# Kernel optimization log

Measured on AMD Instinct MI355X. Metric: run time of the kernel, lower is better.

## Reference

```python
import jax, jax.numpy as jnp
import numpy as np

B, N, IN_DIM, SLOT_DIM, HIDDEN = 32, 4096, 256, 256, 512
NUM_SLOTS, NUM_ITERS = 8, 3
EPS_LN = 1e-5


def layernorm(x, g, b):
    m = jnp.mean(x, axis=-1, keepdims=True)
    v = jnp.var(x, axis=-1, keepdims=True)
    return (x - m) * jax.lax.rsqrt(v + EPS_LN) * g + b


def setup_inputs() -> dict:
    key = jax.random.key(0)
    ks = jax.random.split(key, 16)
    s = 0.02
    return {
        "inputs": jax.random.normal(ks[0], (B, N, IN_DIM), jnp.float32),
        "init_noise": jax.random.normal(ks[1], (B, NUM_SLOTS, SLOT_DIM), jnp.float32),
        "mu": jax.random.normal(ks[2], (1, 1, SLOT_DIM), jnp.float32),
        "sigma_raw": jax.random.normal(ks[3], (1, 1, SLOT_DIM), jnp.float32),
        "ln_in_g": jnp.ones((IN_DIM,), jnp.float32), "ln_in_b": jnp.zeros((IN_DIM,), jnp.float32),
        "ln_s_g": jnp.ones((SLOT_DIM,), jnp.float32), "ln_s_b": jnp.zeros((SLOT_DIM,), jnp.float32),
        "ln_m_g": jnp.ones((SLOT_DIM,), jnp.float32), "ln_m_b": jnp.zeros((SLOT_DIM,), jnp.float32),
        "wq": jax.random.normal(ks[4], (SLOT_DIM, SLOT_DIM), jnp.float32) * s,
        "bq": jnp.zeros((SLOT_DIM,), jnp.float32),
        "wk": jax.random.normal(ks[5], (SLOT_DIM, IN_DIM), jnp.float32) * s,
        "bk": jnp.zeros((SLOT_DIM,), jnp.float32),
        "wv": jax.random.normal(ks[6], (SLOT_DIM, IN_DIM), jnp.float32) * s,
        "bv": jnp.zeros((SLOT_DIM,), jnp.float32),
        "w_ih": jax.random.normal(ks[7], (3 * SLOT_DIM, SLOT_DIM), jnp.float32) * s,
        "w_hh": jax.random.normal(ks[8], (3 * SLOT_DIM, SLOT_DIM), jnp.float32) * s,
        "b_ih": jnp.zeros((3 * SLOT_DIM,), jnp.float32),
        "b_hh": jnp.zeros((3 * SLOT_DIM,), jnp.float32),
        "w1": jax.random.normal(ks[9], (HIDDEN, SLOT_DIM), jnp.float32) * s,
        "b1": jnp.zeros((HIDDEN,), jnp.float32),
        "w2": jax.random.normal(ks[10], (SLOT_DIM, HIDDEN), jnp.float32) * s,
        "b2": jnp.zeros((SLOT_DIM,), jnp.float32),
    }


def gru_cell(x, h, w_ih, w_hh, b_ih, b_hh):
    # PyTorch GRUCell: gates split as (reset, update, new)
    gx = x @ w_ih.T + b_ih
    gh = h @ w_hh.T + b_hh
    xr, xz, xn = jnp.split(gx, 3, axis=-1)
    hr, hz, hn = jnp.split(gh, 3, axis=-1)
    r = jax.nn.sigmoid(xr + hr)
    z = jax.nn.sigmoid(xz + hz)
    n = jnp.tanh(xn + r * hn)
    return (1.0 - z) * n + z * h


def reference(inputs, init_noise, mu, sigma_raw, ln_in_g, ln_in_b, ln_s_g, ln_s_b,
              ln_m_g, ln_m_b, wq, bq, wk, bk, wv, bv, w_ih, w_hh, b_ih, b_hh,
              w1, b1, w2, b2):
    scale = SLOT_DIM ** (-0.5)
    x = layernorm(inputs, ln_in_g, ln_in_b)          # [B,N,Din]
    k = x @ wk.T + bk                                # [B,N,D]
    v = x @ wv.T + bv                                # [B,N,D]
    sigma = jax.nn.softplus(sigma_raw)
    slots = mu + sigma * init_noise                  # [B,S,D]
    attn = None
    for _ in range(NUM_ITERS):
        slots_prev = slots
        q = layernorm(slots, ln_s_g, ln_s_b) @ wq.T + bq      # [B,S,D]
        logits = jnp.einsum('bnd,bsd->bns', k, q) * scale     # [B,N,S]
        attn = jax.nn.softmax(logits, axis=-1) + 1e-8         # softmax over slots
        attn = attn / jnp.sum(attn, axis=1, keepdims=True)    # renorm over inputs
        updates = jnp.einsum('bnd,bns->bsd', v, attn)         # [B,S,D]
        slots = gru_cell(updates, slots_prev, w_ih, w_hh, b_ih, b_hh)
        h = jax.nn.relu(layernorm(slots, ln_m_g, ln_m_b) @ w1.T + b1)
        slots = slots + (h @ w2.T + b2)
    return slots, attn
```

## Files before the change

kernel.cpp:

```cpp
#include <hip/hip_runtime.h>
#include <hip/hip_fp16.h>
#include <cstdint>

#define DEV static __device__ __forceinline__

typedef _Float16 f16x2 __attribute__((ext_vector_type(2)));
typedef _Float16 f16x8 __attribute__((ext_vector_type(8)));
typedef float    f32x4 __attribute__((ext_vector_type(4)));

DEV float fdot2u(uint32_t a, uint32_t b, float c){
  union U { uint32_t u; f16x2 h; };
  U ua; ua.u = a; U ub; ub.u = b;
#if __has_builtin(__builtin_amdgcn_fdot2)
  return __builtin_amdgcn_fdot2(ua.h, ub.h, c, false);
#else
  return c + (float)ua.h[0]*(float)ub.h[0] + (float)ua.h[1]*(float)ub.h[1];
#endif
}

DEV float dot4(uint4 x, uint4 w, float a){
  a = fdot2u(x.x, w.x, a); a = fdot2u(x.y, w.y, a);
  a = fdot2u(x.z, w.z, a); a = fdot2u(x.w, w.w, a);
  return a;
}

DEV float wsum64(float v){
  #pragma unroll
  for (int o = 32; o; o >>= 1) v += __shfl_xor(v, o);
  return v;
}

DEV uint32_t pack2h(float a, float b){
  __half ha = __float2half(a), hb = __float2half(b);
  return (uint32_t)__half_as_ushort(ha) | ((uint32_t)__half_as_ushort(hb) << 16);
}

DEV uint32_t packsh(float v){
  float o = __shfl_xor(v, 1);
  return pack2h(v, o);
}

DEV uint4 packrow8(const float* p){
  uint4 r;
  r.x = pack2h(p[0], p[1]); r.y = pack2h(p[2], p[3]);
  r.z = pack2h(p[4], p[5]); r.w = pack2h(p[6], p[7]);
  return r;
}

__global__ __launch_bounds__(256) void k_lntr(
  const float* __restrict__ xin, const float* __restrict__ lng,
  const float* __restrict__ lnb, uint32_t* __restrict__ xhat,
  const float* __restrict__ wq, const float* __restrict__ wv,
  const float* __restrict__ wih, const float* __restrict__ whh,
  const float* __restrict__ w1, const float* __restrict__ w2,
  const float* __restrict__ wk,
  uint4* __restrict__ WQp4, uint4* __restrict__ WVp4,
  uint4* __restrict__ WIHp4, uint4* __restrict__ WHHp4,
  uint4* __restrict__ W1p4, uint4* __restrict__ W2p4,
  uint4* __restrict__ WKp4)
{
  if (blockIdx.x >= 32768){
    int u = (blockIdx.x - 32768) * 256 + threadIdx.x;
    if (u < 8192){
      int e4 = u >> 8, n = u & 255;
      WVp4[u] = packrow8(wv + n*256 + 8*e4);
    } else if (u < 32768){
      int v = u - 8192; int e4 = v / 768, n = v - e4*768;
      WIHp4[v] = packrow8(wih + n*256 + 8*e4);
    } else if (u < 57344){
      int v = u - 32768; int e4 = v / 768, n = v - e4*768;
      WHHp4[v] = packrow8(whh + n*256 + 8*e4);
    } else if (u < 73728){
      int v = u - 57344; int e4 = v >> 9, n = v & 511;
      W1p4[v] = packrow8(w1 + n*256 + 8*e4);
    } else if (u < 90112){
      int v = u - 73728; int e4 = v >> 8, n = v & 255;
      W2p4[v] = packrow8(w2 + n*512 + 8*e4);
    } else if (u < 98304){
      int v = u - 90112; int e4 = v >> 8, n = v & 255;
      WQp4[v] = packrow8(wq + n*256 + 8*e4);
    } else if (u < 106496){
      int v = u - 98304; int d4 = v >> 8, c = v & 255;
      uint4 r;
      r.x = pack2h(wk[(8*d4+0)*256 + c], wk[(8*d4+1)*256 + c]);
      r.y = pack2h(wk[(8*d4+2)*256 + c], wk[(8*d4+3)*256 + c]);
      r.z = pack2h(wk[(8*d4+4)*256 + c], wk[(8*d4+5)*256 + c]);
      r.w = pack2h(wk[(8*d4+6)*256 + c], wk[(8*d4+7)*256 + c]);
      WKp4[v] = r;
    }
    return;
  }
  int row = blockIdx.x * 4 + (threadIdx.x >> 6);
  int lane = threadIdx.x & 63;
  const float4 xv = ((const float4*)(xin + (size_t)row * 256))[lane];
  float s1 = wsum64(xv.x + xv.y + xv.z + xv.w);
  float s2 = wsum64(xv.x*xv.x + xv.y*xv.y + xv.z*xv.z + xv.w*xv.w);
  float m = s1 * (1.0f/256.0f);
  float var = s2 * (1.0f/256.0f) - m*m;
  float rstd = rsqrtf(var + 1e-5f);
  float4 gv = ((const float4*)lng)[lane];
  float4 bv = ((const float4*)lnb)[lane];
  float y0 = (xv.x - m)*rstd*gv.x + bv.x;
  float y1 = (xv.y - m)*rstd*gv.y + bv.y;
  float y2 = (xv.z - m)*rstd*gv.z + bv.z;
  float y3 = (xv.w - m)*rstd*gv.w + bv.w;
  ((uint2*)(xhat + (size_t)row * 128))[lane] = make_uint2(pack2h(y0,y1), pack2h(y2,y3));
}

template<int MODE>
__global__ __launch_bounds__(512) void k_slot(
  const float* __restrict__ noise, const float* __restrict__ mu,
  const float* __restrict__ sigraw,
  const float* S0, float* SDST,
  const float* __restrict__ UAp, const float* __restrict__ ASp,
  float* __restrict__ AS,
  const uint4* __restrict__ WVp4, const float* __restrict__ bv,
  const uint4* __restrict__ WIHp4, const uint4* __restrict__ WHHp4,
  const float* __restrict__ bih, const float* __restrict__ bhh,
  const float* __restrict__ lmg, const float* __restrict__ lmb,
  const uint4* __restrict__ W1p4, const float* __restrict__ b1,
  const uint4* __restrict__ W2p4, const float* __restrict__ b2,
  const float* __restrict__ lsg, const float* __restrict__ lsb,
  const uint4* __restrict__ WQp4, const float* __restrict__ bq,
  const uint4* __restrict__ WKp4, const float* __restrict__ bk,
  uint32_t* __restrict__ QTH, float* __restrict__ CV)
{
  __shared__ float gx[768], gh[768];
  __shared__ float part[512];
  __shared__ uint4 hs4[32], un4[32], us4[32], sln4[32], q4[32];
  __shared__ uint4 hb4[64];
  __shared__ float redA[8], redB[8];

  const int t = threadIdx.x;
  const int h = t >> 8;
  const int c = t & 255;
  const int lane = t & 63;
  const int w8 = t >> 6;
  const int r = blockIdx.x;
  const int b = r >> 3, s = r & 7;

  float snv = 0.f, spv = 0.f;

  if (MODE == 0){
    if (t < 256){
      float x = sigraw[c];
      float sp = (x > 20.0f) ? x : log1pf(__expf(x));
      snv = mu[c] + sp * noise[r*256 + c];
      SDST[r*256 + c] = snv;
    }
  } else {
    if (w8 == 0){
      float v = (lane < 16) ? ASp[lane*256 + r] : 0.f;
      v += __shfl_xor(v, 1); v += __shfl_xor(v, 2);
      v += __shfl_xor(v, 4); v += __shfl_xor(v, 8);
      if (lane == 0) redA[0] = v;
    }
    __syncthreads();
    const float asum_r = redA[0];
    if (MODE == 2 && t == 0) AS[r] = asum_r;
    const float ainv = 1.0f / asum_r;
    float hv = 0.f;
    if (t < 256){
      hv = S0[r*256 + c];
      float us = 0.f;
      #pragma unroll
      for (int ch = 0; ch < 16; ++ch) us += UAp[ch*65536 + r*256 + c];
      float unv = us * ainv;
      uint32_t ph = packsh(hv), pu = packsh(unv);
      if (!(c & 1)){
        ((uint32_t*)hs4)[c>>1] = ph;
        ((uint32_t*)un4)[c>>1] = pu;
      }
    }
    __syncthreads();

    {
      float a = 0.f;
      #pragma unroll 8
      for (int e4 = h*16; e4 < h*16 + 16; ++e4)
        a = dot4(un4[e4], WVp4[e4*256 + c], a);
      part[t] = a;
    }
    __syncthreads();
    if (t < 256){
      float us = part[t] + part[t + 256] + bv[c];
      uint32_t p = packsh(us);
      if (!(c & 1)) ((uint32_t*)us4)[c>>1] = p;
    }
    __syncthreads();

    {
      const uint4* IN4 = h ? hs4 : us4;
      const uint4* WP = h ? WHHp4 : WIHp4;
      float a0 = 0.f, a1 = 0.f, a2 = 0.f;
      #pragma unroll 8
      for (int e4 = 0; e4 < 32; ++e4){
        uint4 x = IN4[e4];
        a0 = dot4(x, WP[e4*768 + c], a0);
        a1 = dot4(x, WP[e4*768 + 256 + c], a1);
        a2 = dot4(x, WP[e4*768 + 512 + c], a2);
      }
      float* OUT = h ? gh : gx;
      OUT[c] = a0; OUT[256 + c] = a1; OUT[512 + c] = a2;
    }
    __syncthreads();

    if (t < 256){
      float xr = gx[c]     + bih[c];
      float xz = gx[256+c] + bih[256+c];
      float xn = gx[512+c] + bih[512+c];
      float hr = gh[c]     + bhh[c];
      float hz = gh[256+c] + bhh[256+c];
      float hn = gh[512+c] + bhh[512+c];
      float rg = 1.f/(1.f + __expf(-(xr + hr)));
      float zg = 1.f/(1.f + __expf(-(xz + hz)));
      float ng = tanhf(xn + rg*hn);
      spv = (1.f - zg)*ng + zg*hv;
      float a = wsum64(spv), bs = wsum64(spv*spv);
      if (lane == 0){ redA[w8] = a; redB[w8] = bs; }
    }
    __syncthreads();
    {
      float s1 = redA[0]+redA[1]+redA[2]+redA[3];
      float s2 = redB[0]+redB[1]+redB[2]+redB[3];
      float m = s1*(1.f/256.f), var = s2*(1.f/256.f) - m*m;
      float rstd = rsqrtf(var + 1e-5f);
      if (t < 256){
        float slv = (spv - m)*rstd*lmg[c] + lmb[c];
        uint32_t p = packsh(slv);
        if (!(c & 1)) ((uint32_t*)sln4)[c>>1] = p;
      }
    }
    __syncthreads();

    {
      float a = 0.f;
      #pragma unroll 8
      for (int e4 = 0; e4 < 32; ++e4)
        a = dot4(sln4[e4], W1p4[e4*512 + t], a);
      float hval = fmaxf(a + b1[t], 0.f);
      float o = __shfl_xor(hval, 1);
      if (!(t & 1)) ((uint32_t*)hb4)[t>>1] = pack2h(hval, o);
    }
    __syncthreads();

    {
      float a = 0.f;
      #pragma unroll 8
      for (int e4 = h*32; e4 < h*32 + 32; ++e4)
        a = dot4(hb4[e4], W2p4[e4*256 + c], a);
      part[t] = a;
    }
    __syncthreads();
    if (t < 256){
      snv = spv + part[t] + part[t + 256] + b2[c];
      SDST[r*256 + c] = snv;
    }
  }

  if (MODE != 2){
    if (t < 256){
      float a = wsum64(snv), bs = wsum64(snv*snv);
      if (lane == 0){ redA[w8] = a; redB[w8] = bs; }
    }
    __syncthreads();
    {
      float s1 = redA[0]+redA[1]+redA[2]+redA[3];
      float s2 = redB[0]+redB[1]+redB[2]+redB[3];
      float m = s1*(1.f/256.f), var = s2*(1.f/256.f) - m*m;
      float rstd = rsqrtf(var + 1e-5f);
      if (t < 256){
        float slv = (snv - m)*rstd*lsg[c] + lsb[c];
        uint32_t p = packsh(slv);
        if (!(c & 1)) ((uint32_t*)sln4)[c>>1] = p;
      }
    }
    __syncthreads();

    {
      float a = 0.f;
      #pragma unroll 8
      for (int e4 = h*16; e4 < h*16 + 16; ++e4)
        a = dot4(sln4[e4], WQp4[e4*256 + c], a);
      part[t] = a;
    }
    __syncthreads();
    if (t < 256){
      float qv = part[t] + part[t + 256] + bq[c];
      float p = wsum64(bk[c] * qv);
      if (lane == 0) redA[w8] = p;
      uint32_t pk = packsh(qv);
      if (!(c & 1)) ((uint32_t*)q4)[c>>1] = pk;
    }
    __syncthreads();
    {
      float cv = redA[0]+redA[1]+redA[2]+redA[3];
      if (t == 0) CV[r] = cv;
    }

    {
      float a = 0.f;
      #pragma unroll 8
      for (int e4 = h*16; e4 < h*16 + 16; ++e4)
        a = dot4(q4[e4], WKp4[e4*256 + c], a);
      part[t] = a;
    }
    __syncthreads();
    if (t < 256){
      float qtv = part[t] + part[t + 256];
      uint32_t p = packsh(qtv);
      if (!(c & 1)) QTH[b*1024 + (c>>1)*8 + s] = p;
    }
  }
}

template<bool LAST>
__global__ __launch_bounds__(256, 2) void k_attn(
  const uint32_t* __restrict__ xhat,
  const uint32_t* __restrict__ qtpk, const float* __restrict__ cvec,
  float* __restrict__ UAp, float* __restrict__ ASp,
  float* __restrict__ attn_out)
{
  __shared__ uint32_t xs[8192];
  __shared__ uint32_t qs[1024];
  __shared__ float attn_lds[64][16];
  __shared__ float up_lds[8][256];
  __shared__ float as_red[4][8];

  const int b = blockIdx.y, chunk = blockIdx.x;
  const int t = threadIdx.x;
  const int l = t & 63, w = t >> 6;
  const int g = l >> 4, sl = l & 15;

  const size_t base = (size_t)b*4096 + (size_t)chunk*256;

  uint4 stg[8];
  #pragma unroll
  for (int i = 0; i < 8; ++i){
    int c16 = i*256 + t;
    int row = c16 >> 5, q = c16 & 31;
    stg[i] = *(const uint4*)(xhat + (base + row)*128 + q*4);
  }
  for (int i = t; i < 1024; i += 256) qs[i] = qtpk[b*1024 + i];
  #pragma unroll
  for (int i = 0; i < 8; ++i){
    int c16 = i*256 + t;
    int row = c16 >> 5, q = c16 & 31;
    *(uint4*)(xs + row*128 + ((q ^ (row & 7)) << 2)) = stg[i];
  }
  __syncthreads();

  uint4 bq[8];
  #pragma unroll
  for (int kk = 0; kk < 8; ++kk){
    if (sl < 8){
      uint4 v;
      v.x = qs[(16*kk + 4*g + 0)*8 + sl];
      v.y = qs[(16*kk + 4*g + 1)*8 + sl];
      v.z = qs[(16*kk + 4*g + 2)*8 + sl];
      v.w = qs[(16*kk + 4*g + 3)*8 + sl];
      bq[kk] = v;
    } else bq[kk] = make_uint4(0u,0u,0u,0u);
  }
  const float cv = (sl < 8) ? cvec[b*8 + sl] : 0.f;

  float up[8][4];
  #pragma unroll
  for (int s = 0; s < 8; ++s){ up[s][0]=0.f; up[s][1]=0.f; up[s][2]=0.f; up[s][3]=0.f; }
  float asl_acc = 0.f;

  for (int st = 0; st < 4; ++st){
    const int L0 = 16*w;

    f32x4 acc; acc[0]=0.f; acc[1]=0.f; acc[2]=0.f; acc[3]=0.f;
    const int rowA = L0 + sl;
    #pragma unroll
    for (int kk = 0; kk < 8; ++kk){
      uint4 av = *(const uint4*)(xs + rowA*128 + (((4*kk + g) ^ (rowA & 7)) << 2));
      union { uint4 u; f16x8 h; } A, B;
      A.u = av; B.u = bq[kk];
      acc = __builtin_amdgcn_mfma_f32_16x16x32_f16(A.h, B.h, acc, 0, 0, 0);
    }

    #pragma unroll
    for (int reg = 0; reg < 4; ++reg){
      float d = (acc[reg] + cv) * 0.0625f;
      float m = d;
      m = fmaxf(m, __shfl_xor(m, 1));
      m = fmaxf(m, __shfl_xor(m, 2));
      m = fmaxf(m, __shfl_xor(m, 4));
      float e = __expf(d - m);
      float ssum = e;
      ssum += __shfl_xor(ssum, 1);
      ssum += __shfl_xor(ssum, 2);
      ssum += __shfl_xor(ssum, 4);
      float a = e / ssum + 1e-8f;
      asl_acc += a;
      attn_lds[L0 + 4*g + reg][sl] = a;
    }

    if (st < 3){
      const size_t g2 = base + (size_t)(st+1)*64;
      #pragma unroll
      for (int i = 0; i < 8; ++i){
        int c16 = i*256 + t;
        int row = c16 >> 5, q = c16 & 31;
        stg[i] = *(const uint4*)(xhat + (g2 + row)*128 + q*4);
      }
    }

    #pragma unroll 4
    for (int rr = 0; rr < 16; ++rr){
      const int row = L0 + rr;
      const uint32_t* xp = xs + row*128 + ((((l>>1) ^ (row & 7)) << 2) | ((l & 1) << 1));
      uint2 xv = *(const uint2*)xp;
      float x0 = __half2float(__ushort_as_half((unsigned short)(xv.x & 0xffff)));
      float x1 = __half2float(__ushort_as_half((unsigned short)(xv.x >> 16)));
      float x2 = __half2float(__ushort_as_half((unsigned short)(xv.y & 0xffff)));
      float x3 = __half2float(__ushort_as_half((unsigned short)(xv.y >> 16)));
      const float4 a0 = *(const float4*)&attn_lds[row][0];
      const float4 a1 = *(const float4*)&attn_lds[row][4];
      float as8[8] = {a0.x, a0.y, a0.z, a0.w, a1.x, a1.y, a1.z, a1.w};
      #pragma unroll
      for (int s = 0; s < 8; ++s){
        up[s][0] += as8[s]*x0; up[s][1] += as8[s]*x1;
        up[s][2] += as8[s]*x2; up[s][3] += as8[s]*x3;
      }
    }

    if (LAST){
      __syncthreads();
      int row = t >> 2, s0 = (t & 3)*2;
      float2 v = *(const float2*)&attn_lds[row][s0];
      *(float2*)(attn_out + (base + (size_t)st*64 + row)*8 + s0) = v;
    }

    if (st < 3){
      __syncthreads();
      #pragma unroll
      for (int i = 0; i < 8; ++i){
        int c16 = i*256 + t;
        int row = c16 >> 5, q = c16 & 31;
        *(uint4*)(xs + row*128 + ((q ^ (row & 7)) << 2)) = stg[i];
      }
      __syncthreads();
    }
  }

  {
    float v = asl_acc;
    v += __shfl_xor(v, 16);
    v += __shfl_xor(v, 32);
    if (l < 8) as_red[w][l] = v;
  }

  __syncthreads();
  #pragma unroll
  for (int ww = 0; ww < 4; ++ww){
    if (w == ww){
      #pragma unroll
      for (int s = 0; s < 8; ++s){
        float4* dst = (float4*)&up_lds[s][l*4];
        float4 v = make_float4(up[s][0], up[s][1], up[s][2], up[s][3]);
        if (ww){ float4 o = *dst; v.x += o.x; v.y += o.y; v.z += o.z; v.w += o.w; }
        *dst = v;
      }
    }
    __syncthreads();
  }
  #pragma unroll
  for (int s = 0; s < 8; ++s)
    UAp[(size_t)chunk*65536 + (size_t)(b*8 + s)*256 + t] = up_lds[s][t];
  if (t < 8)
    ASp[chunk*256 + b*8 + t] = as_red[0][t] + as_red[1][t] + as_red[2][t] + as_red[3][t];
}

__global__ __launch_bounds__(256) void k_out(
  const float* __restrict__ AS, float* __restrict__ out)
{
  int j = blockIdx.x * 256 + threadIdx.x;
  int b = j >> 15;
  int s = j & 7;
  out[65536 + j] = out[65536 + j] * (1.0f / AS[b*8 + s]);
}

extern "C" void kernel_launch(void* const* d_in, const int* in_sizes, int n_in,
                              void* d_out, int out_size, void* d_ws, size_t ws_size,
                              hipStream_t stream) {
  const float* inputs = (const float*)d_in[0];
  const float* noise  = (const float*)d_in[1];
  const float* mu     = (const float*)d_in[2];
  const float* sigraw = (const float*)d_in[3];
  const float* lng    = (const float*)d_in[4];
  const float* lnb    = (const float*)d_in[5];
  const float* lsg    = (const float*)d_in[6];
  const float* lsb    = (const float*)d_in[7];
  const float* lmg    = (const float*)d_in[8];
  const float* lmb    = (const float*)d_in[9];
  const float* wq     = (const float*)d_in[10];
  const float* bq     = (const float*)d_in[11];
  const float* wk     = (const float*)d_in[12];
  const float* bk     = (const float*)d_in[13];
  const float* wv     = (const float*)d_in[14];
  const float* bv     = (const float*)d_in[15];
  const float* wih    = (const float*)d_in[16];
  const float* whh    = (const float*)d_in[17];
  const float* bih    = (const float*)d_in[18];
  const float* bhh    = (const float*)d_in[19];
  const float* w1     = (const float*)d_in[20];
  const float* b1     = (const float*)d_in[21];
  const float* w2     = (const float*)d_in[22];
  const float* b2     = (const float*)d_in[23];
  float* out = (float*)d_out;

  char* w = (char*)d_ws;
  size_t o = 0;
  uint32_t* XH = (uint32_t*)w;  o += 67108864;
  uint32_t* QT = (uint32_t*)(w + o); o += 131072;
  float* CV  = (float*)(w + o); o += 1024;
  float* AS  = (float*)(w + o); o += 1024;
  float* S0  = (float*)(w + o); o += 262144;
  uint4* WQp = (uint4*)(w + o); o += 131072;
  uint4* WVp = (uint4*)(w + o); o += 131072;
  uint4* WIHp= (uint4*)(w + o); o += 393216;
  uint4* WHHp= (uint4*)(w + o); o += 393216;
  uint4* W1p = (uint4*)(w + o); o += 262144;
  uint4* W2p = (uint4*)(w + o); o += 262144;
  uint4* WKp = (uint4*)(w + o); o += 131072;
  float* UAp = (float*)(w + o); o += 4194304;
  float* ASp = (float*)(w + o); o += 16384;

  k_lntr<<<33184, 256, 0, stream>>>(inputs, lng, lnb, XH,
                                    wq, wv, wih, whh, w1, w2, wk,
                                    WQp, WVp, WIHp, WHHp, W1p, W2p, WKp);
  k_slot<0><<<256, 512, 0, stream>>>(noise, mu, sigraw, S0, S0, UAp, ASp, AS,
      WVp, bv, WIHp, WHHp, bih, bhh, lmg, lmb, W1p, b1, W2p, b2,
      lsg, lsb, WQp, bq, WKp, bk, QT, CV);

  dim3 ga(16, 32);
  for (int it = 0; it < 3; ++it){
    if (it == 2) k_attn<true ><<<ga, 256, 0, stream>>>(XH, QT, CV, UAp, ASp, out + 65536);
    else         k_attn<false><<<ga, 256, 0, stream>>>(XH, QT, CV, UAp, ASp, out + 65536);
    if (it < 2)
      k_slot<1><<<256, 512, 0, stream>>>(noise, mu, sigraw, S0, S0, UAp, ASp, AS,
          WVp, bv, WIHp, WHHp, bih, bhh, lmg, lmb, W1p, b1, W2p, b2,
          lsg, lsb, WQp, bq, WKp, bk, QT, CV);
    else
      k_slot<2><<<256, 512, 0, stream>>>(noise, mu, sigraw, S0, out, UAp, ASp, AS,
          WVp, bv, WIHp, WHHp, bih, bhh, lmg, lmb, W1p, b1, W2p, b2,
          lsg, lsb, WQp, bq, WKp, bk, QT, CV);
  }
  k_out<<<4096, 256, 0, stream>>>(AS, out);
}
```

Before: 410.6 us.

## Load input tiles directly into LDS with global_load_lds instead of register staging

Replaces register-staged prefetch of the xhat tile with direct global-to-LDS 16-byte loads, applying the XOR swizzle on the source column. This frees the staging registers and avoids the extra LDS store pass. However, the next tile is now loaded synchronously between barriers rather than overlapped with compute, and the occupancy hint in launch bounds is dropped.

```diff
diff --git a/kernel.cpp b/kernel.cpp
--- a/kernel.cpp
+++ b/kernel.cpp
@@ -45,6 +45,12 @@
   r.x = pack2h(p[0], p[1]); r.y = pack2h(p[2], p[3]);
   r.z = pack2h(p[4], p[5]); r.w = pack2h(p[6], p[7]);
   return r;
+}
+
+DEV void gld16(const void* g, void* l){
+  __builtin_amdgcn_global_load_lds(
+      (const __attribute__((address_space(1))) void*)g,
+      (__attribute__((address_space(3))) void*)l, 16, 0, 0);
 }
 
 __global__ __launch_bounds__(256) void k_lntr(
@@ -315,7 +321,7 @@
 }
 
 template<bool LAST>
-__global__ __launch_bounds__(256, 2) void k_attn(
+__global__ __launch_bounds__(256) void k_attn(
   const uint32_t* __restrict__ xhat,
   const uint32_t* __restrict__ qtpk, const float* __restrict__ cvec,
   float* __restrict__ UAp, float* __restrict__ ASp,
@@ -334,20 +340,20 @@
 
   const size_t base = (size_t)b*4096 + (size_t)chunk*256;
 
-  uint4 stg[8];
-  #pragma unroll
-  for (int i = 0; i < 8; ++i){
-    int c16 = i*256 + t;
-    int row = c16 >> 5, q = c16 & 31;
-    stg[i] = *(const uint4*)(xhat + (base + row)*128 + q*4);
-  }
   for (int i = t; i < 1024; i += 256) qs[i] = qtpk[b*1024 + i];
-  #pragma unroll
-  for (int i = 0; i < 8; ++i){
-    int c16 = i*256 + t;
-    int row = c16 >> 5, q = c16 & 31;
-    *(uint4*)(xs + row*128 + ((q ^ (row & 7)) << 2)) = stg[i];
-  }
+
+  auto stage = [&](int st){
+    const size_t gr0 = base + (size_t)st*64;
+    #pragma unroll
+    for (int i = 0; i < 8; ++i){
+      int n  = w*8 + i;
+      int rl = 2*n + (l >> 5);
+      int ql = (l & 31) ^ (rl & 7);
+      gld16(xhat + (gr0 + rl)*128 + ql*4, xs + n*256);
+    }
+  };
+
+  stage(0);
   __syncthreads();
 
   uint4 bq[8];
@@ -370,6 +376,7 @@
   float asl_acc = 0.f;
 
   for (int st = 0; st < 4; ++st){
+    if (st){ __syncthreads(); stage(st); __syncthreads(); }
     const int L0 = 16*w;
 
     f32x4 acc; acc[0]=0.f; acc[1]=0.f; acc[2]=0.f; acc[3]=0.f;
@@ -397,16 +404,6 @@
       float a = e / ssum + 1e-8f;
       asl_acc += a;
       attn_lds[L0 + 4*g + reg][sl] = a;
-    }
-
-    if (st < 3){
-      const size_t g2 = base + (size_t)(st+1)*64;
-      #pragma unroll
-      for (int i = 0; i < 8; ++i){
-        int c16 = i*256 + t;
-        int row = c16 >> 5, q = c16 & 31;
-        stg[i] = *(const uint4*)(xhat + (g2 + row)*128 + q*4);
-      }
     }
 
     #pragma unroll 4
@@ -433,17 +430,6 @@
       int row = t >> 2, s0 = (t & 3)*2;
       float2 v = *(const float2*)&attn_lds[row][s0];
       *(float2*)(attn_out + (base + (size_t)st*64 + row)*8 + s0) = v;
-    }
-
-    if (st < 3){
-      __syncthreads();
-      #pragma unroll
-      for (int i = 0; i < 8; ++i){
-        int c16 = i*256 + t;
-        int row = c16 >> 5, q = c16 & 31;
-        *(uint4*)(xs + row*128 + ((q ^ (row & 7)) << 2)) = stg[i];
-      }
-      __syncthreads();
     }
   }
 
```

Result: faster. 373.6 us (-9.0%).
